# Kernel tuning notes

Hardware: AMD Instinct MI355X
Metric: run time of the kernel (lower is better)

Reference implementation:

```python
import jax, jax.numpy as jnp
import numpy as np

N, IN_DIM, H, ATT_DIM, OUT_DIM = 4096, 512, 8, 64, 64
ATT_BIAS = 0.5


def setup_inputs() -> dict:
    key = jax.random.key(0)
    ks = jax.random.split(key, 12)
    s_in = 1.0 / np.sqrt(IN_DIM)
    s_o = 1.0 / np.sqrt(H * OUT_DIM)
    return {
        "Q": jax.random.normal(ks[0], (N, IN_DIM), jnp.float32),
        "K": jax.random.normal(ks[1], (N, IN_DIM), jnp.float32),
        "V": jax.random.normal(ks[2], (N, IN_DIM), jnp.float32),
        "adj": jax.random.uniform(ks[3], (N, N), jnp.float32),
        "WQ": jax.random.normal(ks[4], (IN_DIM, H * ATT_DIM), jnp.float32) * s_in,
        "bQ": jnp.zeros((H * ATT_DIM,), jnp.float32),
        "WK": jax.random.normal(ks[5], (IN_DIM, H * ATT_DIM), jnp.float32) * s_in,
        "bK": jnp.zeros((H * ATT_DIM,), jnp.float32),
        "WV": jax.random.normal(ks[6], (IN_DIM, H * OUT_DIM), jnp.float32) * s_in,
        "bV": jnp.zeros((H * OUT_DIM,), jnp.float32),
        "WO": jax.random.normal(ks[7], (H * OUT_DIM, OUT_DIM), jnp.float32) * s_o,
        "bO": jnp.zeros((OUT_DIM,), jnp.float32),
    }


def reference(Q, K, V, adj, WQ, bQ, WK, bK, WV, bV, WO, bO):
    scale = ATT_DIM ** -0.5
    q = (Q @ WQ + bQ).reshape(N, H, ATT_DIM)   # [N,H,d]
    k = (K @ WK + bK).reshape(N, H, ATT_DIM)   # [N,H,d]
    v = (V @ WV + bV).reshape(N, H, OUT_DIM)   # [N,H,e]
    # scaled QK^T per head: [H,N,N]
    scores = jnp.einsum("nhd,mhd->hnm", q * scale, k)
    # sigmoid -> bias subtract -> +0.1*adj -> softmax over keys
    scores = jax.nn.sigmoid(scores) - ATT_BIAS + 0.1 * adj[None, :, :]
    attn = jax.nn.softmax(scores, axis=2)
    # attend values (dropout p=0 => identity), concat heads, project
    out = jnp.einsum("hnm,mhe->nhe", attn, v).reshape(N, H * OUT_DIM)
    return out @ WO + bO
```

## Files before the change

kernel.cpp:

```cpp
#include <hip/hip_runtime.h>
#include <hip/hip_bf16.h>

#define N_TOK  4096
#define HD     512
#define NH     8
#define NSPLIT 4

typedef short v8s __attribute__((ext_vector_type(8)));
typedef float v4f __attribute__((ext_vector_type(4)));
typedef unsigned short u16;

#define QSCALE   0.18033688011112042f
#define ADJ2     0.14426950408889634f
#define SIG2P    1.4426950408889634f

__device__ __forceinline__ float bf2f(u16 x) {
  union { unsigned int u; float f; } c; c.u = ((unsigned int)x) << 16; return c.f;
}
__device__ __forceinline__ u16 f2bf(float f) {
  union { float f; unsigned int u; } c; c.f = f;
  return (u16)((c.u + 0x7fffu + ((c.u >> 16) & 1u)) >> 16);
}
__device__ __forceinline__ float fast_exp2(float x) {
#if __has_builtin(__builtin_amdgcn_exp2f)
  return __builtin_amdgcn_exp2f(x);
#else
  return exp2f(x);
#endif
}
__device__ __forceinline__ unsigned int pk_bf16(float a, float b) {
  union { __hip_bfloat162 h; unsigned int u; } c;
  c.h = __float22bfloat162_rn(make_float2(a, b));
  return c.u;
}

__global__ void detect_k(const u16* __restrict__ q, int* __restrict__ flag) {
  int l = threadIdx.x;
  u16 e = q[2 * l];
  float x = bf2f(e);
  int ex = (e >> 7) & 0xFF;
  float ax = fabsf(x);
  bool ok = (ex != 0xFF) && (ax < 64.f) && (ax > 1e-30f);
  unsigned long long m = __ballot(ok);
  if (l == 0) *flag = (__popcll(m) >= 48) ? 0 : 1;
}

__global__ __launch_bounds__(256) void conv_adjE_k(const void* __restrict__ adj, u16* __restrict__ adjE,
                                                   const void* sQ, const void* sK, const void* sV, const void* sO,
                                                   u16* dQ, u16* dK, u16* dV, u16* dO,
                                                   const int* __restrict__ flag) {
  int b = blockIdx.x;
  if (b >= 16384) {
    int i = (b - 16384) * 256 + threadIdx.x;
    const void* s; u16* d; int off;
    if (i < 512)       { s = sQ; d = dQ; off = i; }
    else if (i < 1024) { s = sK; d = dK; off = i - 512; }
    else if (i < 1536) { s = sV; d = dV; off = i - 1024; }
    else if (i < 1600) { s = sO; d = dO; off = i - 1536; }
    else return;
    float v = (*flag) ? ((const float*)s)[off] : bf2f(((const u16*)s)[off]);
    d[off] = f2bf(v);
    return;
  }
  int i = b * 256 + threadIdx.x;
  float4 f;
  if (*flag) {
    f = ((const float4*)adj)[i];
  } else {
    short4 v = ((const short4*)adj)[i];
    f.x = bf2f((u16)v.x); f.y = bf2f((u16)v.y); f.z = bf2f((u16)v.z); f.w = bf2f((u16)v.w);
  }
  unsigned int d0 = pk_bf16(fast_exp2(f.x * ADJ2), fast_exp2(f.y * ADJ2));
  unsigned int d1 = pk_bf16(fast_exp2(f.z * ADJ2), fast_exp2(f.w * ADJ2));
  ((uint2*)adjE)[i] = make_uint2(d0, d1);
}

__global__ __launch_bounds__(256) void tr_w_k(const void* W0, const void* W1, const void* W2, const void* W3,
                                              u16* t0, u16* t1, u16* t2, u16* t3,
                                              const int* __restrict__ flag) {
  int z = blockIdx.z;
  const void* in; u16* out; int C;
  if (z == 0)      { in = W0; out = t0; C = 512; }
  else if (z == 1) { in = W1; out = t1; C = 512; }
  else if (z == 2) { in = W2; out = t2; C = 512; }
  else             { in = W3; out = t3; C = 64; if (blockIdx.y) return; }
  const int R = 512;
  __shared__ __align__(16) u16 tile[64][72];
  const int r0 = blockIdx.x * 64, c0 = blockIdx.y * 64;
  const int t = threadIdx.x;
  bool f32 = (*flag) != 0;
#pragma unroll
  for (int rep = 0; rep < 2; ++rep) {
    int idx = (t + rep * 256) * 8;
    int r = idx >> 6, c = idx & 63;
    if (f32) {
      const float* sp = (const float*)in + (size_t)(r0 + r) * C + (c0 + c);
      float4 a = *(const float4*)sp, b = *(const float4*)(sp + 4);
      uint4 q = make_uint4(pk_bf16(a.x, a.y), pk_bf16(a.z, a.w),
                           pk_bf16(b.x, b.y), pk_bf16(b.z, b.w));
      *(uint4*)&tile[r][c] = q;
    } else {
      *(v8s*)&tile[r][c] = *(const v8s*)((const u16*)in + (size_t)(r0 + r) * C + (c0 + c));
    }
  }
  __syncthreads();
#pragma unroll
  for (int rep = 0; rep < 2; ++rep) {
    int idx = (t + rep * 256) * 8;
    int oc = idx >> 6, orr = idx & 63;
    u16 tmp[8];
#pragma unroll
    for (int j = 0; j < 8; ++j) tmp[j] = tile[orr + j][oc];
    *(v8s*)(out + (size_t)(c0 + oc) * R + (r0 + orr)) = *(v8s*)tmp;
  }
}

__global__ __launch_bounds__(256) void tr_bf16(const u16* __restrict__ in, u16* __restrict__ out,
                                               int R, int C) {
  __shared__ __align__(16) u16 tile[64][72];
  const int r0 = blockIdx.x * 64, c0 = blockIdx.y * 64;
  const int t = threadIdx.x;
#pragma unroll
  for (int rep = 0; rep < 2; ++rep) {
    int idx = (t + rep * 256) * 8;
    int r = idx >> 6, c = idx & 63;
    *(v8s*)&tile[r][c] = *(const v8s*)(in + (size_t)(r0 + r) * C + (c0 + c));
  }
  __syncthreads();
#pragma unroll
  for (int rep = 0; rep < 2; ++rep) {
    int idx = (t + rep * 256) * 8;
    int oc = idx >> 6, orr = idx & 63;
    u16 tmp[8];
#pragma unroll
    for (int j = 0; j < 8; ++j) tmp[j] = tile[orr + j][oc];
    *(v8s*)(out + (size_t)(c0 + oc) * R + (r0 + orr)) = *(v8s*)tmp;
  }
}

__global__ __launch_bounds__(256) void gemm_qkv_k(const void* A0, const void* A1, const void* A2,
                                                  const u16* __restrict__ t0, const u16* __restrict__ t1,
                                                  const u16* __restrict__ t2,
                                                  const u16* b0, const u16* b1, const u16* b2,
                                                  u16* o0, u16* o1, u16* o2,
                                                  const int* __restrict__ flag) {
  __shared__ __align__(16) u16 As[64][72];
  __shared__ __align__(16) u16 Bs[64][72];
  int z = blockIdx.z;
  const void* Araw = (z == 0) ? A0 : (z == 1) ? A1 : A2;
  const u16* Bt    = (z == 0) ? t0 : (z == 1) ? t1 : t2;
  const u16* bias  = (z == 0) ? b0 : (z == 1) ? b1 : b2;
  u16* C           = (z == 0) ? o0 : (z == 1) ? o1 : o2;
  const float oscale = (z == 0) ? QSCALE : 1.0f;
  const bool f32 = (*flag) != 0;
  const int i0 = blockIdx.x * 64, j0 = blockIdx.y * 64;
  const int t = threadIdx.x, w = t >> 6, l = t & 63, quad = l >> 4, l15 = l & 15;
  v4f acc[4] = {};
  for (int k0 = 0; k0 < 512; k0 += 64) {
#pragma unroll
    for (int rep = 0; rep < 2; ++rep) {
      int idx = (t + rep * 256) * 8;
      int r = idx >> 6, c = idx & 63;
      if (f32) {
        const float* sp = (const float*)Araw + (size_t)(i0 + r) * 512 + k0 + c;
        float4 fa = *(const float4*)sp, fb = *(const float4*)(sp + 4);
        uint4 q = make_uint4(pk_bf16(fa.x, fa.y), pk_bf16(fa.z, fa.w),
                             pk_bf16(fb.x, fb.y), pk_bf16(fb.z, fb.w));
        *(uint4*)&As[r][c] = q;
      } else {
        *(v8s*)&As[r][c] = *(const v8s*)((const u16*)Araw + (size_t)(i0 + r) * 512 + k0 + c);
      }
      *(v8s*)&Bs[r][c] = *(const v8s*)(Bt + (size_t)(j0 + r) * 512 + k0 + c);
    }
    __syncthreads();
#pragma unroll
    for (int h = 0; h < 2; ++h) {
      v8s a = *(const v8s*)&As[w * 16 + l15][h * 32 + quad * 8];
#pragma unroll
      for (int cb = 0; cb < 4; ++cb) {
        v8s b = *(const v8s*)&Bs[cb * 16 + l15][h * 32 + quad * 8];
        acc[cb] = __builtin_amdgcn_mfma_f32_16x16x32_bf16(a, b, acc[cb], 0, 0, 0);
      }
    }
    __syncthreads();
  }
#pragma unroll
  for (int cb = 0; cb < 4; ++cb) {
    int col = j0 + cb * 16 + l15;
    float bv = bf2f(bias[col]);
#pragma unroll
    for (int r = 0; r < 4; ++r) {
      int row = i0 + w * 16 + quad * 4 + r;
      C[(size_t)row * HD + col] = f2bf((acc[cb][r] + bv) * oscale);
    }
  }
}

__global__ __launch_bounds__(256) void gemm_bt(const u16* __restrict__ A, const u16* __restrict__ Bt,
                                               const u16* __restrict__ bias, void* __restrict__ C,
                                               const int* __restrict__ outflag, int NB, int K) {
  __shared__ __align__(16) u16 As[64][72];
  __shared__ __align__(16) u16 Bs[64][72];
  const int i0 = blockIdx.x * 64, j0 = blockIdx.y * 64;
  const int t = threadIdx.x, w = t >> 6, l = t & 63, quad = l >> 4, l15 = l & 15;
  v4f acc[4] = {};
  for (int k0 = 0; k0 < K; k0 += 64) {
#pragma unroll
    for (int rep = 0; rep < 2; ++rep) {
      int idx = (t + rep * 256) * 8;
      int r = idx >> 6, c = idx & 63;
      *(v8s*)&As[r][c] = *(const v8s*)(A + (size_t)(i0 + r) * K + k0 + c);
      *(v8s*)&Bs[r][c] = *(const v8s*)(Bt + (size_t)(j0 + r) * K + k0 + c);
    }
    __syncthreads();
#pragma unroll
    for (int h = 0; h < 2; ++h) {
      v8s a = *(const v8s*)&As[w * 16 + l15][h * 32 + quad * 8];
#pragma unroll
      for (int cb = 0; cb < 4; ++cb) {
        v8s b = *(const v8s*)&Bs[cb * 16 + l15][h * 32 + quad * 8];
        acc[cb] = __builtin_amdgcn_mfma_f32_16x16x32_bf16(a, b, acc[cb], 0, 0, 0);
      }
    }
    __syncthreads();
  }
  bool f32o = (*outflag) != 0;
#pragma unroll
  for (int cb = 0; cb < 4; ++cb) {
    int col = j0 + cb * 16 + l15;
    float bv = bf2f(bias[col]);
#pragma unroll
    for (int r = 0; r < 4; ++r) {
      int row = i0 + w * 16 + quad * 4 + r;
      float v = acc[cb][r] + bv;
      size_t idx = (size_t)row * NB + col;
      if (f32o) ((float*)C)[idx] = v;
      else      ((u16*)C)[idx] = f2bf(v);
    }
  }
}

__global__ __launch_bounds__(256, 5) void attn_kernel(const u16* __restrict__ qb, const u16* __restrict__ kb,
                                                      const u16* __restrict__ vtb, const u16* __restrict__ adjE,
                                                      u16* __restrict__ Opart, float* __restrict__ Lpart) {
  __shared__ __align__(16) u16 Ks[64][72];
  __shared__ __align__(16) u16 Vs[64][72];
  __shared__ __align__(16) u16 Ps[4][16][72];
  const int i0 = blockIdx.x * 64, h64 = blockIdx.y * 64, z = blockIdx.z;
  const int t = threadIdx.x, w = t >> 6, l = t & 63, quad = l >> 4, l15 = l & 15;
  const int iRow = i0 + w * 16 + l15;

  v8s qf[2];
#pragma unroll
  for (int h = 0; h < 2; ++h)
    qf[h] = *(const v8s*)(qb + (size_t)iRow * HD + h64 + h * 32 + quad * 8);

  const u16* adjRow = adjE + (size_t)iRow * N_TOK;
  v4f oacc[4] = {};
  float lsum = 0.f;

  const int m_begin = z * (N_TOK / NSPLIT);
  for (int m0 = m_begin; m0 < m_begin + N_TOK / NSPLIT; m0 += 64) {
    uint2 av[4];
#pragma unroll
    for (int cb = 0; cb < 4; ++cb)
      av[cb] = *(const uint2*)(adjRow + m0 + cb * 16 + quad * 4);

#pragma unroll
    for (int rep = 0; rep < 2; ++rep) {
      int idx = (t + rep * 256) * 8;
      int r = idx >> 6, c = idx & 63;
      *(v8s*)&Ks[r][c] = *(const v8s*)(kb  + (size_t)(m0 + r) * HD + h64 + c);
      *(v8s*)&Vs[r][c] = *(const v8s*)(vtb + (size_t)(h64 + r) * N_TOK + m0 + c);
    }
    __syncthreads();

    v4f s[4] = {};
#pragma unroll
    for (int h = 0; h < 2; ++h) {
#pragma unroll
      for (int cb = 0; cb < 4; ++cb) {
        v8s kf = *(const v8s*)&Ks[cb * 16 + l15][h * 32 + quad * 8];
        s[cb] = __builtin_amdgcn_mfma_f32_16x16x32_bf16(kf, qf[h], s[cb], 0, 0, 0);
      }
    }

#pragma unroll
    for (int cb = 0; cb < 4; ++cb) {
      union { unsigned int u; float f; } e0, e1, e2, e3;
      e0.u = av[cb].x << 16; e1.u = av[cb].x & 0xFFFF0000u;
      e2.u = av[cb].y << 16; e3.u = av[cb].y & 0xFFFF0000u;
      float p0, p1, p2, p3;
      {
        float u0 = fast_exp2(-s[cb][0]); p0 = fast_exp2(__builtin_amdgcn_rcpf(1.f + u0) * SIG2P) * e0.f;
        float u1 = fast_exp2(-s[cb][1]); p1 = fast_exp2(__builtin_amdgcn_rcpf(1.f + u1) * SIG2P) * e1.f;
        float u2 = fast_exp2(-s[cb][2]); p2 = fast_exp2(__builtin_amdgcn_rcpf(1.f + u2) * SIG2P) * e2.f;
        float u3 = fast_exp2(-s[cb][3]); p3 = fast_exp2(__builtin_amdgcn_rcpf(1.f + u3) * SIG2P) * e3.f;
      }
      lsum += (p0 + p1) + (p2 + p3);
      *(uint2*)&Ps[w][l15][cb * 16 + quad * 4] = make_uint2(pk_bf16(p0, p1), pk_bf16(p2, p3));
    }
    asm volatile("s_waitcnt lgkmcnt(0)" ::: "memory");

#pragma unroll
    for (int h = 0; h < 2; ++h) {
      v8s pa = *(const v8s*)&Ps[w][l15][h * 32 + quad * 8];
#pragma unroll
      for (int eb = 0; eb < 4; ++eb) {
        v8s vf = *(const v8s*)&Vs[eb * 16 + l15][h * 32 + quad * 8];
        oacc[eb] = __builtin_amdgcn_mfma_f32_16x16x32_bf16(pa, vf, oacc[eb], 0, 0, 0);
      }
    }
    __syncthreads();
  }

  lsum += __shfl_xor(lsum, 16);
  lsum += __shfl_xor(lsum, 32);
  if (l < 16)
    Lpart[((size_t)z * N_TOK + i0 + w * 16 + l) * NH + blockIdx.y] = lsum;
#pragma unroll
  for (int eb = 0; eb < 4; ++eb) {
#pragma unroll
    for (int r = 0; r < 4; ++r) {
      size_t row = (size_t)z * N_TOK + i0 + w * 16 + quad * 4 + r;
      Opart[row * HD + h64 + eb * 16 + l15] = f2bf(oacc[eb][r]);
    }
  }
}

__global__ __launch_bounds__(256) void reduce_k(const u16* __restrict__ Opart, const float* __restrict__ Lpart,
                                                u16* __restrict__ ab) {
  int i = blockIdx.x * 256 + threadIdx.x;
  int row = i >> 7;
  int c4 = i & 127;
  int h = c4 >> 4;
  float lv = 0.f;
#pragma unroll
  for (int s = 0; s < NSPLIT; ++s) lv += Lpart[((size_t)s * N_TOK + row) * NH + h];
  float ax = 0.f, ay = 0.f, az = 0.f, aw = 0.f;
#pragma unroll
  for (int s = 0; s < NSPLIT; ++s) {
    short4 v = ((const short4*)Opart)[(size_t)s * (N_TOK * HD / 4) + i];
    ax += bf2f((u16)v.x); ay += bf2f((u16)v.y); az += bf2f((u16)v.z); aw += bf2f((u16)v.w);
  }
  float rl = __builtin_amdgcn_rcpf(lv);
  ((uint2*)ab)[i] = make_uint2(pk_bf16(ax * rl, ay * rl), pk_bf16(az * rl, aw * rl));
}

extern "C" void kernel_launch(void* const* d_in, const int* in_sizes, int n_in,
                              void* d_out, int out_size, void* d_ws, size_t ws_size,
                              hipStream_t stream) {
  (void)in_sizes; (void)n_in; (void)out_size; (void)ws_size;
  const void* Q   = d_in[0];
  const void* K   = d_in[1];
  const void* V   = d_in[2];
  const void* adj = d_in[3];
  const void* WQ  = d_in[4];
  const void* bQ  = d_in[5];
  const void* WK  = d_in[6];
  const void* bK  = d_in[7];
  const void* WV  = d_in[8];
  const void* bV  = d_in[9];
  const void* WO  = d_in[10];
  const void* bO  = d_in[11];

  char* p = (char*)d_ws;
  auto alloc = [&](size_t bytes) { char* r = p; p += (bytes + 255) & ~(size_t)255; return r; };
  const size_t SZ = (size_t)N_TOK * HD * 2;

  int* flag    = (int*)alloc(256);
  u16* adjE    = (u16*)alloc((size_t)N_TOK * N_TOK * 2);
  u16* qb      = (u16*)alloc(SZ);
  u16* kb      = (u16*)alloc(SZ);
  u16* vb      = (u16*)alloc(SZ);
  u16* vtb     = (u16*)alloc(SZ);
  u16* ab      = (u16*)alloc(SZ);
  u16* Opart   = (u16*)alloc((size_t)NSPLIT * SZ);
  float* Lpart = (float*)alloc((size_t)NSPLIT * N_TOK * NH * 4);
  u16* tQ      = (u16*)alloc((size_t)512 * 512 * 2);
  u16* tK      = (u16*)alloc((size_t)512 * 512 * 2);
  u16* tV      = (u16*)alloc((size_t)512 * 512 * 2);
  u16* tO      = (u16*)alloc((size_t)64 * 512 * 2);
  u16* bQc     = (u16*)alloc(512 * 2);
  u16* bKc     = (u16*)alloc(512 * 2);
  u16* bVc     = (u16*)alloc(512 * 2);
  u16* bOc     = (u16*)alloc(64 * 2);

  dim3 b256(256);
  detect_k<<<1, 64, 0, stream>>>((const u16*)Q, flag);

  conv_adjE_k<<<dim3(16384 + 7), b256, 0, stream>>>(adj, adjE, bQ, bK, bV, bO,
                                                    bQc, bKc, bVc, bOc, flag);
  tr_w_k<<<dim3(8, 8, 4), b256, 0, stream>>>(WQ, WK, WV, WO, tQ, tK, tV, tO, flag);

  gemm_qkv_k<<<dim3(64, 8, 3), b256, 0, stream>>>(Q, K, V, tQ, tK, tV,
                                                  bQc, bKc, bVc, qb, kb, vb, flag);

  tr_bf16<<<dim3(64, 8), b256, 0, stream>>>(vb, vtb, N_TOK, HD);

  attn_kernel<<<dim3(N_TOK / 64, NH, NSPLIT), b256, 0, stream>>>(qb, kb, vtb, adjE, Opart, Lpart);

  reduce_k<<<dim3(N_TOK * HD / 4 / 256), b256, 0, stream>>>(Opart, Lpart, ab);

  gemm_bt<<<dim3(64, 1), b256, 0, stream>>>(ab, tO, bOc, d_out, flag, 64, 512);
}
```

Before: 274.2 us.

## Fuse detect, bias, transpose and reduce stages; read K/V fragments directly from global

Removes the separate dtype-detect kernel: each kernel now recomputes the check inline, and biases are read straight from the inputs. The V projection writes its output already transposed via swapped MFMA operands, which drops the tr_bf16 kernel. The split-K reduction is folded into the output-projection GEMM's A-tile load, and the attention kernel loads K and V fragments directly from global memory instead of staging them in LDS, with no block barriers left in the loop. The goal is fewer launches and less intermediate traffic, at the risk of uncoalesced global fragment loads in attention, a slow strided transposed store, and a lower occupancy hint (5 to 4).

```diff
diff --git a/kernel.cpp b/kernel.cpp
--- a/kernel.cpp
+++ b/kernel.cpp
@@ -34,37 +34,26 @@
   return c.u;
 }
 
-__global__ void detect_k(const u16* __restrict__ q, int* __restrict__ flag) {
-  int l = threadIdx.x;
+__device__ __forceinline__ bool detect_f32(const u16* __restrict__ q) {
+  int l = threadIdx.x & 63;
   u16 e = q[2 * l];
   float x = bf2f(e);
   int ex = (e >> 7) & 0xFF;
   float ax = fabsf(x);
   bool ok = (ex != 0xFF) && (ax < 64.f) && (ax > 1e-30f);
   unsigned long long m = __ballot(ok);
-  if (l == 0) *flag = (__popcll(m) >= 48) ? 0 : 1;
+  return __popcll(m) < 48;
+}
+__device__ __forceinline__ float bias_ld(const void* b, int i, bool f32) {
+  return f32 ? ((const float*)b)[i] : bf2f(((const u16*)b)[i]);
 }
 
 __global__ __launch_bounds__(256) void conv_adjE_k(const void* __restrict__ adj, u16* __restrict__ adjE,
-                                                   const void* sQ, const void* sK, const void* sV, const void* sO,
-                                                   u16* dQ, u16* dK, u16* dV, u16* dO,
-                                                   const int* __restrict__ flag) {
-  int b = blockIdx.x;
-  if (b >= 16384) {
-    int i = (b - 16384) * 256 + threadIdx.x;
-    const void* s; u16* d; int off;
-    if (i < 512)       { s = sQ; d = dQ; off = i; }
-    else if (i < 1024) { s = sK; d = dK; off = i - 512; }
-    else if (i < 1536) { s = sV; d = dV; off = i - 1024; }
-    else if (i < 1600) { s = sO; d = dO; off = i - 1536; }
-    else return;
-    float v = (*flag) ? ((const float*)s)[off] : bf2f(((const u16*)s)[off]);
-    d[off] = f2bf(v);
-    return;
-  }
-  int i = b * 256 + threadIdx.x;
+                                                   const u16* __restrict__ Qdet) {
+  bool f32 = detect_f32(Qdet);
+  int i = blockIdx.x * 256 + threadIdx.x;
   float4 f;
-  if (*flag) {
+  if (f32) {
     f = ((const float4*)adj)[i];
   } else {
     short4 v = ((const short4*)adj)[i];
@@ -77,7 +66,8 @@
 
 __global__ __launch_bounds__(256) void tr_w_k(const void* W0, const void* W1, const void* W2, const void* W3,
                                               u16* t0, u16* t1, u16* t2, u16* t3,
-                                              const int* __restrict__ flag) {
+                                              const u16* __restrict__ Qdet) {
+  bool f32 = detect_f32(Qdet);
   int z = blockIdx.z;
   const void* in; u16* out; int C;
   if (z == 0)      { in = W0; out = t0; C = 512; }
@@ -88,7 +78,6 @@
   __shared__ __align__(16) u16 tile[64][72];
   const int r0 = blockIdx.x * 64, c0 = blockIdx.y * 64;
   const int t = threadIdx.x;
-  bool f32 = (*flag) != 0;
 #pragma unroll
   for (int rep = 0; rep < 2; ++rep) {
     int idx = (t + rep * 256) * 8;
@@ -115,44 +104,20 @@
   }
 }
 
-__global__ __launch_bounds__(256) void tr_bf16(const u16* __restrict__ in, u16* __restrict__ out,
-                                               int R, int C) {
-  __shared__ __align__(16) u16 tile[64][72];
-  const int r0 = blockIdx.x * 64, c0 = blockIdx.y * 64;
-  const int t = threadIdx.x;
-#pragma unroll
-  for (int rep = 0; rep < 2; ++rep) {
-    int idx = (t + rep * 256) * 8;
-    int r = idx >> 6, c = idx & 63;
-    *(v8s*)&tile[r][c] = *(const v8s*)(in + (size_t)(r0 + r) * C + (c0 + c));
-  }
-  __syncthreads();
-#pragma unroll
-  for (int rep = 0; rep < 2; ++rep) {
-    int idx = (t + rep * 256) * 8;
-    int oc = idx >> 6, orr = idx & 63;
-    u16 tmp[8];
-#pragma unroll
-    for (int j = 0; j < 8; ++j) tmp[j] = tile[orr + j][oc];
-    *(v8s*)(out + (size_t)(c0 + oc) * R + (r0 + orr)) = *(v8s*)tmp;
-  }
-}
-
 __global__ __launch_bounds__(256) void gemm_qkv_k(const void* A0, const void* A1, const void* A2,
                                                   const u16* __restrict__ t0, const u16* __restrict__ t1,
                                                   const u16* __restrict__ t2,
-                                                  const u16* b0, const u16* b1, const u16* b2,
-                                                  u16* o0, u16* o1, u16* o2,
-                                                  const int* __restrict__ flag) {
+                                                  const void* b0, const void* b1, const void* b2,
+                                                  u16* __restrict__ qb, u16* __restrict__ kb,
+                                                  u16* __restrict__ vtb) {
   __shared__ __align__(16) u16 As[64][72];
   __shared__ __align__(16) u16 Bs[64][72];
+  bool f32 = detect_f32((const u16*)A0);
   int z = blockIdx.z;
   const void* Araw = (z == 0) ? A0 : (z == 1) ? A1 : A2;
   const u16* Bt    = (z == 0) ? t0 : (z == 1) ? t1 : t2;
-  const u16* bias  = (z == 0) ? b0 : (z == 1) ? b1 : b2;
-  u16* C           = (z == 0) ? o0 : (z == 1) ? o1 : o2;
-  const float oscale = (z == 0) ? QSCALE : 1.0f;
-  const bool f32 = (*flag) != 0;
+  const void* bias = (z == 0) ? b0 : (z == 1) ? b1 : b2;
+  const bool vt = (z == 2);
   const int i0 = blockIdx.x * 64, j0 = blockIdx.y * 64;
   const int t = threadIdx.x, w = t >> 6, l = t & 63, quad = l >> 4, l15 = l & 15;
   v4f acc[4] = {};
@@ -173,78 +138,58 @@
       *(v8s*)&Bs[r][c] = *(const v8s*)(Bt + (size_t)(j0 + r) * 512 + k0 + c);
     }
     __syncthreads();
-#pragma unroll
-    for (int h = 0; h < 2; ++h) {
-      v8s a = *(const v8s*)&As[w * 16 + l15][h * 32 + quad * 8];
-#pragma unroll
-      for (int cb = 0; cb < 4; ++cb) {
-        v8s b = *(const v8s*)&Bs[cb * 16 + l15][h * 32 + quad * 8];
-        acc[cb] = __builtin_amdgcn_mfma_f32_16x16x32_bf16(a, b, acc[cb], 0, 0, 0);
+    if (vt) {
+#pragma unroll
+      for (int h = 0; h < 2; ++h) {
+        v8s a = *(const v8s*)&As[w * 16 + l15][h * 32 + quad * 8];
+#pragma unroll
+        for (int cb = 0; cb < 4; ++cb) {
+          v8s b = *(const v8s*)&Bs[cb * 16 + l15][h * 32 + quad * 8];
+          acc[cb] = __builtin_amdgcn_mfma_f32_16x16x32_bf16(b, a, acc[cb], 0, 0, 0);
+        }
+      }
+    } else {
+#pragma unroll
+      for (int h = 0; h < 2; ++h) {
+        v8s a = *(const v8s*)&As[w * 16 + l15][h * 32 + quad * 8];
+#pragma unroll
+        for (int cb = 0; cb < 4; ++cb) {
+          v8s b = *(const v8s*)&Bs[cb * 16 + l15][h * 32 + quad * 8];
+          acc[cb] = __builtin_amdgcn_mfma_f32_16x16x32_bf16(a, b, acc[cb], 0, 0, 0);
+        }
       }
     }
     __syncthreads();
   }
-#pragma unroll
-  for (int cb = 0; cb < 4; ++cb) {
-    int col = j0 + cb * 16 + l15;
-    float bv = bf2f(bias[col]);
-#pragma unroll
-    for (int r = 0; r < 4; ++r) {
-      int row = i0 + w * 16 + quad * 4 + r;
-      C[(size_t)row * HD + col] = f2bf((acc[cb][r] + bv) * oscale);
-    }
-  }
-}
-
-__global__ __launch_bounds__(256) void gemm_bt(const u16* __restrict__ A, const u16* __restrict__ Bt,
-                                               const u16* __restrict__ bias, void* __restrict__ C,
-                                               const int* __restrict__ outflag, int NB, int K) {
-  __shared__ __align__(16) u16 As[64][72];
-  __shared__ __align__(16) u16 Bs[64][72];
-  const int i0 = blockIdx.x * 64, j0 = blockIdx.y * 64;
-  const int t = threadIdx.x, w = t >> 6, l = t & 63, quad = l >> 4, l15 = l & 15;
-  v4f acc[4] = {};
-  for (int k0 = 0; k0 < K; k0 += 64) {
-#pragma unroll
-    for (int rep = 0; rep < 2; ++rep) {
-      int idx = (t + rep * 256) * 8;
-      int r = idx >> 6, c = idx & 63;
-      *(v8s*)&As[r][c] = *(const v8s*)(A + (size_t)(i0 + r) * K + k0 + c);
-      *(v8s*)&Bs[r][c] = *(const v8s*)(Bt + (size_t)(j0 + r) * K + k0 + c);
-    }
-    __syncthreads();
-#pragma unroll
-    for (int h = 0; h < 2; ++h) {
-      v8s a = *(const v8s*)&As[w * 16 + l15][h * 32 + quad * 8];
-#pragma unroll
-      for (int cb = 0; cb < 4; ++cb) {
-        v8s b = *(const v8s*)&Bs[cb * 16 + l15][h * 32 + quad * 8];
-        acc[cb] = __builtin_amdgcn_mfma_f32_16x16x32_bf16(a, b, acc[cb], 0, 0, 0);
-      }
-    }
-    __syncthreads();
-  }
-  bool f32o = (*outflag) != 0;
-#pragma unroll
-  for (int cb = 0; cb < 4; ++cb) {
-    int col = j0 + cb * 16 + l15;
-    float bv = bf2f(bias[col]);
-#pragma unroll
-    for (int r = 0; r < 4; ++r) {
-      int row = i0 + w * 16 + quad * 4 + r;
-      float v = acc[cb][r] + bv;
-      size_t idx = (size_t)row * NB + col;
-      if (f32o) ((float*)C)[idx] = v;
-      else      ((u16*)C)[idx] = f2bf(v);
-    }
-  }
-}
-
-__global__ __launch_bounds__(256, 5) void attn_kernel(const u16* __restrict__ qb, const u16* __restrict__ kb,
+  if (vt) {
+#pragma unroll
+    for (int cb = 0; cb < 4; ++cb) {
+#pragma unroll
+      for (int r = 0; r < 4; ++r) {
+        int jj = j0 + cb * 16 + quad * 4 + r;
+        int ii = i0 + w * 16 + l15;
+        vtb[(size_t)jj * N_TOK + ii] = f2bf(acc[cb][r] + bias_ld(bias, jj, f32));
+      }
+    }
+  } else {
+    const float oscale = (z == 0) ? QSCALE : 1.0f;
+    u16* C = (z == 0) ? qb : kb;
+#pragma unroll
+    for (int cb = 0; cb < 4; ++cb) {
+      int col = j0 + cb * 16 + l15;
+      float bv = bias_ld(bias, col, f32);
+#pragma unroll
+      for (int r = 0; r < 4; ++r) {
+        int row = i0 + w * 16 + quad * 4 + r;
+        C[(size_t)row * HD + col] = f2bf((acc[cb][r] + bv) * oscale);
+      }
+    }
+  }
+}
+
+__global__ __launch_bounds__(256, 4) void attn_kernel(const u16* __restrict__ qb, const u16* __restrict__ kb,
                                                       const u16* __restrict__ vtb, const u16* __restrict__ adjE,
                                                       u16* __restrict__ Opart, float* __restrict__ Lpart) {
-  __shared__ __align__(16) u16 Ks[64][72];
-  __shared__ __align__(16) u16 Vs[64][72];
   __shared__ __align__(16) u16 Ps[4][16][72];
   const int i0 = blockIdx.x * 64, h64 = blockIdx.y * 64, z = blockIdx.z;
   const int t = threadIdx.x, w = t >> 6, l = t & 63, quad = l >> 4, l15 = l & 15;
@@ -266,21 +211,12 @@
     for (int cb = 0; cb < 4; ++cb)
       av[cb] = *(const uint2*)(adjRow + m0 + cb * 16 + quad * 4);
 
-#pragma unroll
-    for (int rep = 0; rep < 2; ++rep) {
-      int idx = (t + rep * 256) * 8;
-      int r = idx >> 6, c = idx & 63;
-      *(v8s*)&Ks[r][c] = *(const v8s*)(kb  + (size_t)(m0 + r) * HD + h64 + c);
-      *(v8s*)&Vs[r][c] = *(const v8s*)(vtb + (size_t)(h64 + r) * N_TOK + m0 + c);
-    }
-    __syncthreads();
-
     v4f s[4] = {};
 #pragma unroll
     for (int h = 0; h < 2; ++h) {
 #pragma unroll
       for (int cb = 0; cb < 4; ++cb) {
-        v8s kf = *(const v8s*)&Ks[cb * 16 + l15][h * 32 + quad * 8];
+        v8s kf = *(const v8s*)(kb + (size_t)(m0 + cb * 16 + l15) * HD + h64 + h * 32 + quad * 8);
         s[cb] = __builtin_amdgcn_mfma_f32_16x16x32_bf16(kf, qf[h], s[cb], 0, 0, 0);
       }
     }
@@ -290,13 +226,10 @@
       union { unsigned int u; float f; } e0, e1, e2, e3;
       e0.u = av[cb].x << 16; e1.u = av[cb].x & 0xFFFF0000u;
       e2.u = av[cb].y << 16; e3.u = av[cb].y & 0xFFFF0000u;
-      float p0, p1, p2, p3;
-      {
-        float u0 = fast_exp2(-s[cb][0]); p0 = fast_exp2(__builtin_amdgcn_rcpf(1.f + u0) * SIG2P) * e0.f;
-        float u1 = fast_exp2(-s[cb][1]); p1 = fast_exp2(__builtin_amdgcn_rcpf(1.f + u1) * SIG2P) * e1.f;
-        float u2 = fast_exp2(-s[cb][2]); p2 = fast_exp2(__builtin_amdgcn_rcpf(1.f + u2) * SIG2P) * e2.f;
-        float u3 = fast_exp2(-s[cb][3]); p3 = fast_exp2(__builtin_amdgcn_rcpf(1.f + u3) * SIG2P) * e3.f;
-      }
+      float u0 = fast_exp2(-s[cb][0]); float p0 = fast_exp2(__builtin_amdgcn_rcpf(1.f + u0) * SIG2P) * e0.f;
+      float u1 = fast_exp2(-s[cb][1]); float p1 = fast_exp2(__builtin_amdgcn_rcpf(1.f + u1) * SIG2P) * e1.f;
+      float u2 = fast_exp2(-s[cb][2]); float p2 = fast_exp2(__builtin_amdgcn_rcpf(1.f + u2) * SIG2P) * e2.f;
+      float u3 = fast_exp2(-s[cb][3]); float p3 = fast_exp2(__builtin_amdgcn_rcpf(1.f + u3) * SIG2P) * e3.f;
       lsum += (p0 + p1) + (p2 + p3);
       *(uint2*)&Ps[w][l15][cb * 16 + quad * 4] = make_uint2(pk_bf16(p0, p1), pk_bf16(p2, p3));
     }
@@ -307,11 +240,10 @@
       v8s pa = *(const v8s*)&Ps[w][l15][h * 32 + quad * 8];
 #pragma unroll
       for (int eb = 0; eb < 4; ++eb) {
-        v8s vf = *(const v8s*)&Vs[eb * 16 + l15][h * 32 + quad * 8];
+        v8s vf = *(const v8s*)(vtb + (size_t)(h64 + eb * 16 + l15) * N_TOK + m0 + h * 32 + quad * 8);
         oacc[eb] = __builtin_amdgcn_mfma_f32_16x16x32_bf16(pa, vf, oacc[eb], 0, 0, 0);
       }
     }
-    __syncthreads();
   }
 
   lsum += __shfl_xor(lsum, 16);
@@ -328,23 +260,62 @@
   }
 }
 
-__global__ __launch_bounds__(256) void reduce_k(const u16* __restrict__ Opart, const float* __restrict__ Lpart,
-                                                u16* __restrict__ ab) {
-  int i = blockIdx.x * 256 + threadIdx.x;
-  int row = i >> 7;
-  int c4 = i & 127;
-  int h = c4 >> 4;
-  float lv = 0.f;
-#pragma unroll
-  for (int s = 0; s < NSPLIT; ++s) lv += Lpart[((size_t)s * N_TOK + row) * NH + h];
-  float ax = 0.f, ay = 0.f, az = 0.f, aw = 0.f;
-#pragma unroll
-  for (int s = 0; s < NSPLIT; ++s) {
-    short4 v = ((const short4*)Opart)[(size_t)s * (N_TOK * HD / 4) + i];
-    ax += bf2f((u16)v.x); ay += bf2f((u16)v.y); az += bf2f((u16)v.z); aw += bf2f((u16)v.w);
-  }
-  float rl = __builtin_amdgcn_rcpf(lv);
-  ((uint2*)ab)[i] = make_uint2(pk_bf16(ax * rl, ay * rl), pk_bf16(az * rl, aw * rl));
+__global__ __launch_bounds__(256) void gemm_bt(const u16* __restrict__ Opart, const float* __restrict__ Lpart,
+                                               const u16* __restrict__ Bt, const void* bias,
+                                               void* __restrict__ C, const u16* __restrict__ Qdet) {
+  __shared__ __align__(16) u16 As[64][72];
+  __shared__ __align__(16) u16 Bs[64][72];
+  bool f32 = detect_f32(Qdet);
+  const int i0 = blockIdx.x * 64;
+  const int t = threadIdx.x, w = t >> 6, l = t & 63, quad = l >> 4, l15 = l & 15;
+  v4f acc[4] = {};
+  for (int k0 = 0; k0 < 512; k0 += 64) {
+    const int h = k0 >> 6;
+#pragma unroll
+    for (int rep = 0; rep < 2; ++rep) {
+      int idx = (t + rep * 256) * 8;
+      int r = idx >> 6, c = idx & 63;
+      float lv = 0.f;
+#pragma unroll
+      for (int s = 0; s < NSPLIT; ++s) lv += Lpart[((size_t)s * N_TOK + i0 + r) * NH + h];
+      float rl = __builtin_amdgcn_rcpf(lv);
+      float vals[8] = {};
+#pragma unroll
+      for (int s = 0; s < NSPLIT; ++s) {
+        v8s ov = *(const v8s*)(Opart + ((size_t)s * N_TOK + i0 + r) * HD + k0 + c);
+#pragma unroll
+        for (int j = 0; j < 8; ++j) vals[j] += bf2f((u16)ov[j]);
+      }
+      uint4 q = make_uint4(pk_bf16(vals[0] * rl, vals[1] * rl), pk_bf16(vals[2] * rl, vals[3] * rl),
+                           pk_bf16(vals[4] * rl, vals[5] * rl), pk_bf16(vals[6] * rl, vals[7] * rl));
+      *(uint4*)&As[r][c] = q;
+      *(v8s*)&Bs[r][c] = *(const v8s*)(Bt + (size_t)r * 512 + k0 + c);
+    }
+    __syncthreads();
+#pragma unroll
+    for (int h2 = 0; h2 < 2; ++h2) {
+      v8s a = *(const v8s*)&As[w * 16 + l15][h2 * 32 + quad * 8];
+#pragma unroll
+      for (int cb = 0; cb < 4; ++cb) {
+        v8s b = *(const v8s*)&Bs[cb * 16 + l15][h2 * 32 + quad * 8];
+        acc[cb] = __builtin_amdgcn_mfma_f32_16x16x32_bf16(a, b, acc[cb], 0, 0, 0);
+      }
+    }
+    __syncthreads();
+  }
+#pragma unroll
+  for (int cb = 0; cb < 4; ++cb) {
+    int col = cb * 16 + l15;
+    float bv = bias_ld(bias, col, f32);
+#pragma unroll
+    for (int r = 0; r < 4; ++r) {
+      int row = i0 + w * 16 + quad * 4 + r;
+      float v = acc[cb][r] + bv;
+      size_t idx = (size_t)row * 64 + col;
+      if (f32) ((float*)C)[idx] = v;
+      else     ((u16*)C)[idx] = f2bf(v);
+    }
+  }
 }
 
 extern "C" void kernel_launch(void* const* d_in, const int* in_sizes, int n_in,
@@ -363,44 +334,28 @@
   const void* bV  = d_in[9];
   const void* WO  = d_in[10];
   const void* bO  = d_in[11];
+  const u16* Qdet = (const u16*)Q;
 
   char* p = (char*)d_ws;
   auto alloc = [&](size_t bytes) { char* r = p; p += (bytes + 255) & ~(size_t)255; return r; };
   const size_t SZ = (size_t)N_TOK * HD * 2;
 
-  int* flag    = (int*)alloc(256);
   u16* adjE    = (u16*)alloc((size_t)N_TOK * N_TOK * 2);
   u16* qb      = (u16*)alloc(SZ);
   u16* kb      = (u16*)alloc(SZ);
-  u16* vb      = (u16*)alloc(SZ);
   u16* vtb     = (u16*)alloc(SZ);
-  u16* ab      = (u16*)alloc(SZ);
   u16* Opart   = (u16*)alloc((size_t)NSPLIT * SZ);
   float* Lpart = (float*)alloc((size_t)NSPLIT * N_TOK * NH * 4);
   u16* tQ      = (u16*)alloc((size_t)512 * 512 * 2);
   u16* tK      = (u16*)alloc((size_t)512 * 512 * 2);
   u16* tV      = (u16*)alloc((size_t)512 * 512 * 2);
   u16* tO      = (u16*)alloc((size_t)64 * 512 * 2);
-  u16* bQc     = (u16*)alloc(512 * 2);
-  u16* bKc     = (u16*)alloc(512 * 2);
-  u16* bVc     = (u16*)alloc(512 * 2);
-  u16* bOc     = (u16*)alloc(64 * 2);
 
   dim3 b256(256);
-  detect_k<<<1, 64, 0, stream>>>((const u16*)Q, flag);
-
-  conv_adjE_k<<<dim3(16384 + 7), b256, 0, stream>>>(adj, adjE, bQ, bK, bV, bO,
-                                                    bQc, bKc, bVc, bOc, flag);
-  tr_w_k<<<dim3(8, 8, 4), b256, 0, stream>>>(WQ, WK, WV, WO, tQ, tK, tV, tO, flag);
-
+  conv_adjE_k<<<dim3(16384), b256, 0, stream>>>(adj, adjE, Qdet);
+  tr_w_k<<<dim3(8, 8, 4), b256, 0, stream>>>(WQ, WK, WV, WO, tQ, tK, tV, tO, Qdet);
   gemm_qkv_k<<<dim3(64, 8, 3), b256, 0, stream>>>(Q, K, V, tQ, tK, tV,
-                                                  bQc, bKc, bVc, qb, kb, vb, flag);
-
-  tr_bf16<<<dim3(64, 8), b256, 0, stream>>>(vb, vtb, N_TOK, HD);
-
+                                                  bQ, bK, bV, qb, kb, vtb);
   attn_kernel<<<dim3(N_TOK / 64, NH, NSPLIT), b256, 0, stream>>>(qb, kb, vtb, adjE, Opart, Lpart);
-
-  reduce_k<<<dim3(N_TOK * HD / 4 / 256), b256, 0, stream>>>(Opart, Lpart, ab);
-
-  gemm_bt<<<dim3(64, 1), b256, 0, stream>>>(ab, tO, bOc, d_out, flag, 64, 512);
-}
+  gemm_bt<<<dim3(64, 1), b256, 0, stream>>>(Opart, Lpart, tO, bO, d_out, Qdet);
+}
```

Measured after the change: 470.4 us. 1.72x slower.
